# Optimization experiments

Hardware: AMD Instinct MI355X
Metric: run time of the kernel (lower is better)

Reference implementation:

```python
import jax, jax.numpy as jnp
import numpy as np
import math

B, C_IN, C_QK, H, W, NH = 1, 256, 128, 96, 96, 8
SCALE = math.sqrt(C_QK / NH)  # sqrt(planes/num_head) = 4.0
TEMP = 1.0


def conv1x1(x, w, b=None):
    # x: [B, Cin, H, W], w: [Cout, Cin] -> [B, Cout, H, W]
    y = jnp.einsum('bchw,oc->bohw', x, w)
    if b is not None:
        y = y + b[None, :, None, None]
    return y


def maxpool2x2(x):
    return jax.lax.reduce_window(x, -jnp.inf, jax.lax.max,
                                 (1, 1, 2, 2), (1, 1, 2, 2), 'VALID')


def setup_inputs() -> dict:
    key = jax.random.key(0)
    ks = jax.random.split(key, 5)
    x = jax.random.normal(ks[0], (B, C_IN, H, W), dtype=jnp.float32)
    # conv weights: init.normal_(w, 0, 0.01), zero bias; conv_value has no bias
    w_q = jax.random.normal(ks[1], (C_QK, C_IN), dtype=jnp.float32) * 0.01
    b_q = jnp.zeros((C_QK,), dtype=jnp.float32)
    w_k = jax.random.normal(ks[2], (C_QK, C_IN), dtype=jnp.float32) * 0.01
    b_k = jnp.zeros((C_QK,), dtype=jnp.float32)
    w_v = jax.random.normal(ks[3], (C_IN, C_IN), dtype=jnp.float32) * 0.01
    return {'x': x, 'w_q': w_q, 'b_q': b_q, 'w_k': w_k, 'b_k': b_k, 'w_v': w_v}


def reference(x, w_q, b_q, w_k, b_k, w_v):
    residual = x
    input_x = maxpool2x2(x)                       # [B, Cin, H/2, W/2]
    Hd, Wd = H // 2, W // 2
    Nq, Nk = H * W, Hd * Wd

    q = conv1x1(x, w_q, b_q)                      # [B, Cqk, H, W]
    k = conv1x1(input_x, w_k, b_k)                # [B, Cqk, Hd, Wd]
    v = conv1x1(input_x, w_v)                     # [B, Cin, Hd, Wd]

    dq = C_QK // NH
    dv = C_IN // NH
    q = q.reshape(B * NH, dq, Nq)
    k = k.reshape(B * NH, dq, Nk)
    v = v.reshape(B * NH, dv, Nk)

    # dot distance: scaled by sqrt(planes/num_head) and temp (nowd empty)
    sim = jnp.einsum('bdq,bdk->bqk', q, k) / (SCALE * TEMP)
    attn = jax.nn.softmax(sim, axis=2)            # softmax over keys

    # out = value @ attn^T  -> [B*NH, dv, Nq]
    out = jnp.einsum('bdk,bqk->bdq', v, attn)
    out = out.reshape(B, C_IN, H, W)
    return out + residual
```

## Files before the change

kernel.cpp:

```cpp
#include <hip/hip_runtime.h>
#include <hip/hip_bf16.h>
#include <math.h>

#define C_IN   256
#define C_QK   128
#define NH     8
#define H_     96
#define W_     96
#define NQ     (H_*W_)
#define HD     48
#define WD     48
#define NK     (HD*WD)
#define DQ     16
#define DV     32
#define NQC    (NQ/32)
#define NKC    (NK/32)
#define QPAIRS (NQC/2)
#define KQRT   (NKC/4)
#define KSTEPS (C_IN/16)
#define QS     0.3606737602222409f

typedef __attribute__((ext_vector_type(8)))  short short8v;
typedef __attribute__((ext_vector_type(16))) float f32x16;
typedef __attribute__((ext_vector_type(2)))  int   v2i;

union B8u { uint u[4]; short8v v; };

static __device__ inline ushort bf16r(float f) {
    __hip_bfloat16 h = __float2bfloat16(f);
    return *reinterpret_cast<ushort*>(&h);
}
static __device__ inline uint cvtpk(float lo, float hi) {
    uint r;
    asm("v_cvt_pk_bf16_f32 %0, %1, %2" : "=v"(r) : "v"(lo), "v"(hi));
    return r;
}
static __device__ inline void lswap(uint a, uint b, uint& x, uint& y, int hi) {
#if __has_builtin(__builtin_amdgcn_permlane32_swap)
    v2i r = __builtin_amdgcn_permlane32_swap((int)a, (int)b, false, false);
    x = (uint)r.x;
    y = (uint)r.y;
#else
    uint bx = (uint)__shfl_xor((int)b, 32);
    uint ax = (uint)__shfl_xor((int)a, 32);
    x = hi ? bx : a;
    y = hi ? b : ax;
#endif
}
static __device__ inline float fexp2(float v) {
#if __has_builtin(__builtin_amdgcn_exp2f)
    return __builtin_amdgcn_exp2f(v);
#else
    return __expf(v * 0.6931471805599453f);
#endif
}

#define U_XB   (NQC*KSTEPS*64)
#define U_XPB  (NKC*KSTEPS*64)
#define U_WQ   (4*KSTEPS*64)
#define U_WK   (4*KSTEPS*64)
#define U_WV   (8*KSTEPS*64)
#define U_FRAG (U_XB+U_XPB+U_WQ+U_WK+U_WV)
#define U_TOT  (U_FRAG + 128)

__global__ __launch_bounds__(256) void prep_kernel(
    const float* __restrict__ x,  const float* __restrict__ wq, const float* __restrict__ bq,
    const float* __restrict__ wk, const float* __restrict__ wv,
    ushort* __restrict__ xbP, ushort* __restrict__ xpbP,
    ushort* __restrict__ wqP, ushort* __restrict__ wkP, ushort* __restrict__ wvP,
    float* __restrict__ bqs)
{
    int t = blockIdx.x * 256 + threadIdx.x;
    if (t >= U_TOT) return;
    if (t >= U_FRAG) { int i = t - U_FRAG; bqs[i] = bq[i] * QS; return; }

    union { ushort s[8]; uint4 v; } ou;
    int u = t;
    if (u < U_XB) {
        int l = u & 63, rest = u >> 6;
        int ks = rest & 15, nc = rest >> 4;
        int n  = nc * 32 + (l & 31);
        int k0 = ks * 16 + 8 * (l >> 5);
        #pragma unroll
        for (int j = 0; j < 8; ++j) ou.s[j] = bf16r(x[(size_t)(k0 + j) * NQ + n]);
        *(uint4*)&xbP[(size_t)u * 8] = ou.v;
        return;
    }
    u -= U_XB;
    if (u < U_XPB) {
        int l = u & 63, rest = u >> 6;
        int ks = rest & 15, nc = rest >> 4;
        int np = nc * 32 + (l & 31);
        int k0 = ks * 16 + 8 * (l >> 5);
        int py = np / WD, px = np - py * WD;
        const float* base = x + (2 * py) * W_ + 2 * px;
        #pragma unroll
        for (int j = 0; j < 8; ++j) {
            const float* p = base + (size_t)(k0 + j) * NQ;
            ou.s[j] = bf16r(fmaxf(fmaxf(p[0], p[1]), fmaxf(p[W_], p[W_ + 1])));
        }
        *(uint4*)&xpbP[(size_t)u * 8] = ou.v;
        return;
    }
    u -= U_XPB;
    if (u < U_WQ) {
        int l = u & 63, ks = (u >> 6) & 15, mb = u >> 10;
        int m = mb * 32 + (l & 31), k0 = ks * 16 + 8 * (l >> 5);
        #pragma unroll
        for (int j = 0; j < 8; ++j) ou.s[j] = bf16r(wq[m * C_IN + k0 + j] * QS);
        *(uint4*)&wqP[(size_t)u * 8] = ou.v;
        return;
    }
    u -= U_WQ;
    if (u < U_WK) {
        int l = u & 63, ks = (u >> 6) & 15, mb = u >> 10;
        int m = mb * 32 + (l & 31), k0 = ks * 16 + 8 * (l >> 5);
        #pragma unroll
        for (int j = 0; j < 8; ++j) ou.s[j] = bf16r(wk[m * C_IN + k0 + j]);
        *(uint4*)&wkP[(size_t)u * 8] = ou.v;
        return;
    }
    u -= U_WK;
    {
        int l = u & 63, ks = (u >> 6) & 15, cb = u >> 10;
        int c = cb * 32 + (l & 31), k0 = ks * 16 + 8 * (l >> 5);
        #pragma unroll
        for (int j = 0; j < 8; ++j) ou.s[j] = bf16r(wv[c * C_IN + k0 + j]);
        *(uint4*)&wvP[(size_t)u * 8] = ou.v;
    }
}

static __device__ inline f32x16 mfma_loop(const ushort* __restrict__ A,
                                          const ushort* __restrict__ B) {
    f32x16 acc;
    #pragma unroll
    for (int r = 0; r < 16; ++r) acc[r] = 0.0f;
    #pragma unroll
    for (int s = 0; s < KSTEPS; ++s) {
        short8v a = *(const short8v*)(A + (size_t)s * 512);
        short8v b = *(const short8v*)(B + (size_t)s * 512);
        acc = __builtin_amdgcn_mfma_f32_32x32x16_bf16(a, b, acc, 0, 0, 0);
    }
    return acc;
}
static __device__ inline void xform(const f32x16& acc, int hi, short8v& F1, short8v& F2) {
    uint a0 = cvtpk(acc[0],  acc[1]),  a1 = cvtpk(acc[2],  acc[3]);
    uint b0 = cvtpk(acc[4],  acc[5]),  b1 = cvtpk(acc[6],  acc[7]);
    uint a2 = cvtpk(acc[8],  acc[9]),  a3 = cvtpk(acc[10], acc[11]);
    uint b2 = cvtpk(acc[12], acc[13]), b3 = cvtpk(acc[14], acc[15]);
    B8u f1, f2;
    lswap(a0, b0, f1.u[0], f1.u[2], hi);
    lswap(a1, b1, f1.u[1], f1.u[3], hi);
    lswap(a2, b2, f2.u[0], f2.u[2], hi);
    lswap(a3, b3, f2.u[1], f2.u[3], hi);
    F1 = f1.v; F2 = f2.v;
}

#define T_Q 1152
#define T_K (T_Q + 288)
#define T_ALL (T_K + 576)

__global__ __launch_bounds__(256) void gemm_fused(
    const ushort* __restrict__ xbP, const ushort* __restrict__ xpbP,
    const ushort* __restrict__ wqP, const ushort* __restrict__ wkP,
    const ushort* __restrict__ wvP,
    const float* __restrict__ bqs, const float* __restrict__ bk,
    ushort* __restrict__ qpack, ushort* __restrict__ kpack, ushort* __restrict__ vpack)
{
    int lane = threadIdx.x & 63, wvi = threadIdx.x >> 6;
    int hi = lane >> 5;
    int t = blockIdx.x * 4 + wvi;
    if (t >= T_ALL) return;

    if (t < T_Q) {
        int mb = t / NQC, nc = t - mb * NQC;
        const ushort* A = wqP + ((size_t)(mb * KSTEPS) * 64 + lane) * 8;
        const ushort* B = xbP + ((size_t)(nc * KSTEPS) * 64 + lane) * 8;
        f32x16 acc = mfma_loop(A, B);
        #pragma unroll
        for (int r = 0; r < 16; ++r)
            acc[r] += bqs[mb * 32 + (r & 3) + 8 * (r >> 2) + 4 * hi];
        short8v F1, F2;
        xform(acc, hi, F1, F2);
        *(short8v*)&qpack[((size_t)((2 * mb)     * NQC + nc) * 64 + lane) * 8] = F1;
        *(short8v*)&qpack[((size_t)((2 * mb + 1) * NQC + nc) * 64 + lane) * 8] = F2;
    } else if (t < T_K) {
        int t2 = t - T_Q;
        int mb = t2 / NKC, nc = t2 - mb * NKC;
        const ushort* A = wkP  + ((size_t)(mb * KSTEPS) * 64 + lane) * 8;
        const ushort* B = xpbP + ((size_t)(nc * KSTEPS) * 64 + lane) * 8;
        f32x16 acc = mfma_loop(A, B);
        #pragma unroll
        for (int r = 0; r < 16; ++r)
            acc[r] += bk[mb * 32 + (r & 3) + 8 * (r >> 2) + 4 * hi];
        short8v F1, F2;
        xform(acc, hi, F1, F2);
        *(short8v*)&kpack[((size_t)((2 * mb)     * NKC + nc) * 64 + lane) * 8] = F1;
        *(short8v*)&kpack[((size_t)((2 * mb + 1) * NKC + nc) * 64 + lane) * 8] = F2;
    } else {
        int t3 = t - T_K;
        int cb = t3 / NKC, kc = t3 - cb * NKC;
        const ushort* A = xpbP + ((size_t)(kc * KSTEPS) * 64 + lane) * 8;
        const ushort* B = wvP  + ((size_t)(cb * KSTEPS) * 64 + lane) * 8;
        f32x16 acc = mfma_loop(A, B);
        short8v F1, F2;
        xform(acc, hi, F1, F2);
        *(short8v*)&vpack[((size_t)((cb * NKC + kc) * 2 + 0) * 64 + lane) * 8] = F1;
        *(short8v*)&vpack[((size_t)((cb * NKC + kc) * 2 + 1) * 64 + lane) * 8] = F2;
    }
}

__global__ __launch_bounds__(256, 4) void attn_kernel(const ushort* __restrict__ qpack,
                                                      const ushort* __restrict__ kpack,
                                                      const ushort* __restrict__ vpack,
                                                      const float* __restrict__ x,
                                                      float* __restrict__ out) {
    __shared__ float part[4][2][64][20];
    const int h = blockIdx.y;
    const int tid = threadIdx.x, lane = tid & 63;
    const int kh = tid >> 6;
    const int q31 = lane & 31, hi = lane >> 5;
    const int qp = blockIdx.x;

    short8v qf0 = *(const short8v*)&qpack[((size_t)(h * NQC + 2 * qp)     * 64 + lane) * 8];
    short8v qf1 = *(const short8v*)&qpack[((size_t)(h * NQC + 2 * qp + 1) * 64 + lane) * 8];

    const ushort* kp = kpack + ((size_t)(h * NKC + kh * KQRT) * 64 + lane) * 8;
    const ushort* vp = vpack + ((size_t)(h * NKC + kh * KQRT) * 2 * 64 + lane) * 8;

    short8v kf = *(const short8v*)kp;
    short8v v0 = *(const short8v*)vp;
    short8v v1 = *(const short8v*)(vp + 512);

    f32x16 o0, o1, zc;
    #pragma unroll
    for (int r = 0; r < 16; ++r) { o0[r] = 0.0f; o1[r] = 0.0f; zc[r] = 0.0f; }
    float rs0 = 0.0f, rs1 = 0.0f;

    for (int c = 0; c < KQRT; ++c) {
        short8v kcur = kf, v0c = v0, v1c = v1;
        int cn = (c == KQRT - 1) ? 0 : (c + 1);
        kf = *(const short8v*)(kp + (size_t)cn * 512);
        v0 = *(const short8v*)(vp + (size_t)cn * 1024);
        v1 = *(const short8v*)(vp + (size_t)cn * 1024 + 512);

        {
            f32x16 s = __builtin_amdgcn_mfma_f32_32x32x16_bf16(kcur, qf0, zc, 0, 0, 0);
            float e[16];
            #pragma unroll
            for (int r = 0; r < 16; ++r) e[r] = fexp2(s[r]);
            float t0 = 0.0f;
            #pragma unroll
            for (int r = 0; r < 16; ++r) t0 += e[r];
            rs0 += t0;
            uint a0 = cvtpk(e[0],  e[1]),  a1 = cvtpk(e[2],  e[3]);
            uint b0 = cvtpk(e[4],  e[5]),  b1 = cvtpk(e[6],  e[7]);
            uint a2 = cvtpk(e[8],  e[9]),  a3 = cvtpk(e[10], e[11]);
            uint b2 = cvtpk(e[12], e[13]), b3 = cvtpk(e[14], e[15]);
            B8u B1, B2;
            lswap(a0, b0, B1.u[0], B1.u[2], hi);
            lswap(a1, b1, B1.u[1], B1.u[3], hi);
            lswap(a2, b2, B2.u[0], B2.u[2], hi);
            lswap(a3, b3, B2.u[1], B2.u[3], hi);
            o0 = __builtin_amdgcn_mfma_f32_32x32x16_bf16(v0c, B1.v, o0, 0, 0, 0);
            o0 = __builtin_amdgcn_mfma_f32_32x32x16_bf16(v1c, B2.v, o0, 0, 0, 0);
        }
        {
            f32x16 s = __builtin_amdgcn_mfma_f32_32x32x16_bf16(kcur, qf1, zc, 0, 0, 0);
            float e[16];
            #pragma unroll
            for (int r = 0; r < 16; ++r) e[r] = fexp2(s[r]);
            float t0 = 0.0f;
            #pragma unroll
            for (int r = 0; r < 16; ++r) t0 += e[r];
            rs1 += t0;
            uint a0 = cvtpk(e[0],  e[1]),  a1 = cvtpk(e[2],  e[3]);
            uint b0 = cvtpk(e[4],  e[5]),  b1 = cvtpk(e[6],  e[7]);
            uint a2 = cvtpk(e[8],  e[9]),  a3 = cvtpk(e[10], e[11]);
            uint b2 = cvtpk(e[12], e[13]), b3 = cvtpk(e[14], e[15]);
            B8u B1, B2;
            lswap(a0, b0, B1.u[0], B1.u[2], hi);
            lswap(a1, b1, B1.u[1], B1.u[3], hi);
            lswap(a2, b2, B2.u[0], B2.u[2], hi);
            lswap(a3, b3, B2.u[1], B2.u[3], hi);
            o1 = __builtin_amdgcn_mfma_f32_32x32x16_bf16(v0c, B1.v, o1, 0, 0, 0);
            o1 = __builtin_amdgcn_mfma_f32_32x32x16_bf16(v1c, B2.v, o1, 0, 0, 0);
        }
    }

    rs0 += __shfl_xor(rs0, 32);
    rs1 += __shfl_xor(rs1, 32);

    {
        float* p0 = &part[kh][0][lane][0];
        #pragma unroll
        for (int i = 0; i < 4; ++i)
            *(float4*)&p0[4 * i] = *(float4*)((const float*)&o0 + 4 * i);
        p0[16] = rs0;
        float* p1 = &part[kh][1][lane][0];
        #pragma unroll
        for (int i = 0; i < 4; ++i)
            *(float4*)&p1[4 * i] = *(float4*)((const float*)&o1 + 4 * i);
        p1[16] = rs1;
    }
    __syncthreads();

    if (kh < 2) {
        float o[16] = {};
        float rs = 0.0f;
        #pragma unroll
        for (int w = 0; w < 4; ++w) {
            const float* pw = &part[w][kh][lane][0];
            #pragma unroll
            for (int i = 0; i < 4; ++i) {
                float4 f = *(const float4*)&pw[4 * i];
                o[4 * i + 0] += f.x; o[4 * i + 1] += f.y;
                o[4 * i + 2] += f.z; o[4 * i + 3] += f.w;
            }
            rs += pw[16];
        }
        float inv = 1.0f / rs;
        int q = (2 * qp + kh) * 32 + q31;
        #pragma unroll
        for (int r = 0; r < 16; ++r) {
            int dv = (r & 3) + 8 * (r >> 2) + 4 * hi;
            size_t i0 = (size_t)(h * DV + dv) * NQ + q;
            out[i0] = o[r] * inv + x[i0];
        }
    }
}

extern "C" void kernel_launch(void* const* d_in, const int* in_sizes, int n_in,
                              void* d_out, int out_size, void* d_ws, size_t ws_size,
                              hipStream_t stream) {
    const float* x  = (const float*)d_in[0];
    const float* wq = (const float*)d_in[1];
    const float* bq = (const float*)d_in[2];
    const float* wk = (const float*)d_in[3];
    const float* bk = (const float*)d_in[4];
    const float* wv = (const float*)d_in[5];
    float* out = (float*)d_out;

    ushort* p = (ushort*)d_ws;
    ushort* xbP   = p;  p += (size_t)U_XB  * 8;
    ushort* xpbP  = p;  p += (size_t)U_XPB * 8;
    ushort* wqP   = p;  p += (size_t)U_WQ  * 8;
    ushort* wkP   = p;  p += (size_t)U_WK  * 8;
    ushort* wvP   = p;  p += (size_t)U_WV  * 8;
    ushort* qpack = p;  p += (size_t)NH * NQC * 64 * 8;
    ushort* kpack = p;  p += (size_t)NH * NKC * 64 * 8;
    ushort* vpack = p;  p += (size_t)NH * NKC * 2 * 64 * 8;
    float*  bqs   = (float*)p;

    prep_kernel<<<(U_TOT + 255) / 256, 256, 0, stream>>>(x, wq, bq, wk, wv,
                                                         xbP, xpbP, wqP, wkP, wvP, bqs);
    gemm_fused<<<(T_ALL + 3) / 4, 256, 0, stream>>>(xbP, xpbP, wqP, wkP, wvP,
                                                    bqs, bk, qpack, kpack, vpack);
    attn_kernel<<<dim3(QPAIRS, NH), 256, 0, stream>>>(qpack, kpack, vpack, x, out);
}
```

Baseline: 105.8 us.

## Fuse x bf16 conversion into Q projection and trim attention register pressure

The prep kernel no longer builds a packed bf16 copy of the full-resolution input. The Q-projection path in the fused GEMM now reads fp32 x directly, converts it to bf16 in registers and feeds the MFMA, which removes one full write and read of the input tensor. The attention kernel is also restructured: each softmax step is split into two half-batches of exponentials, the second value fragment is loaded inside the loop instead of prefetched, and the minimum-occupancy hint on the launch bounds is dropped. These attention changes aim to cut register pressure, but the v1 load now sits on the critical path, and the Q GEMM's strided fp32 loads may coalesce less well.

```diff
diff --git a/kernel.cpp b/kernel.cpp
--- a/kernel.cpp
+++ b/kernel.cpp
@@ -55,18 +55,17 @@
 #endif
 }
 
-#define U_XB   (NQC*KSTEPS*64)
 #define U_XPB  (NKC*KSTEPS*64)
 #define U_WQ   (4*KSTEPS*64)
 #define U_WK   (4*KSTEPS*64)
 #define U_WV   (8*KSTEPS*64)
-#define U_FRAG (U_XB+U_XPB+U_WQ+U_WK+U_WV)
+#define U_FRAG (U_XPB+U_WQ+U_WK+U_WV)
 #define U_TOT  (U_FRAG + 128)
 
 __global__ __launch_bounds__(256) void prep_kernel(
     const float* __restrict__ x,  const float* __restrict__ wq, const float* __restrict__ bq,
     const float* __restrict__ wk, const float* __restrict__ wv,
-    ushort* __restrict__ xbP, ushort* __restrict__ xpbP,
+    ushort* __restrict__ xpbP,
     ushort* __restrict__ wqP, ushort* __restrict__ wkP, ushort* __restrict__ wvP,
     float* __restrict__ bqs)
 {
@@ -76,17 +75,6 @@
 
     union { ushort s[8]; uint4 v; } ou;
     int u = t;
-    if (u < U_XB) {
-        int l = u & 63, rest = u >> 6;
-        int ks = rest & 15, nc = rest >> 4;
-        int n  = nc * 32 + (l & 31);
-        int k0 = ks * 16 + 8 * (l >> 5);
-        #pragma unroll
-        for (int j = 0; j < 8; ++j) ou.s[j] = bf16r(x[(size_t)(k0 + j) * NQ + n]);
-        *(uint4*)&xbP[(size_t)u * 8] = ou.v;
-        return;
-    }
-    u -= U_XB;
     if (u < U_XPB) {
         int l = u & 63, rest = u >> 6;
         int ks = rest & 15, nc = rest >> 4;
@@ -161,7 +149,7 @@
 #define T_ALL (T_K + 576)
 
 __global__ __launch_bounds__(256) void gemm_fused(
-    const ushort* __restrict__ xbP, const ushort* __restrict__ xpbP,
+    const float* __restrict__ x, const ushort* __restrict__ xpbP,
     const ushort* __restrict__ wqP, const ushort* __restrict__ wkP,
     const ushort* __restrict__ wvP,
     const float* __restrict__ bqs, const float* __restrict__ bk,
@@ -175,8 +163,21 @@
     if (t < T_Q) {
         int mb = t / NQC, nc = t - mb * NQC;
         const ushort* A = wqP + ((size_t)(mb * KSTEPS) * 64 + lane) * 8;
-        const ushort* B = xbP + ((size_t)(nc * KSTEPS) * 64 + lane) * 8;
-        f32x16 acc = mfma_loop(A, B);
+        const float* xb = x + (size_t)(8 * hi) * NQ + nc * 32 + (lane & 31);
+        f32x16 acc;
+        #pragma unroll
+        for (int r = 0; r < 16; ++r) acc[r] = 0.0f;
+        #pragma unroll
+        for (int s = 0; s < KSTEPS; ++s) {
+            float f[8];
+            #pragma unroll
+            for (int j = 0; j < 8; ++j) f[j] = xb[(size_t)(s * 16 + j) * NQ];
+            B8u bf;
+            #pragma unroll
+            for (int m = 0; m < 4; ++m) bf.u[m] = cvtpk(f[2 * m], f[2 * m + 1]);
+            short8v a = *(const short8v*)(A + (size_t)s * 512);
+            acc = __builtin_amdgcn_mfma_f32_32x32x16_bf16(a, bf.v, acc, 0, 0, 0);
+        }
         #pragma unroll
         for (int r = 0; r < 16; ++r)
             acc[r] += bqs[mb * 32 + (r & 3) + 8 * (r >> 2) + 4 * hi];
@@ -210,11 +211,38 @@
     }
 }
 
-__global__ __launch_bounds__(256, 4) void attn_kernel(const ushort* __restrict__ qpack,
-                                                      const ushort* __restrict__ kpack,
-                                                      const ushort* __restrict__ vpack,
-                                                      const float* __restrict__ x,
-                                                      float* __restrict__ out) {
+static __device__ inline void qstep(short8v kcur, short8v qf, short8v v0c, short8v v1c,
+                                    f32x16& o, float& rs, const f32x16& zc, int hi) {
+    f32x16 s = __builtin_amdgcn_mfma_f32_32x32x16_bf16(kcur, qf, zc, 0, 0, 0);
+    {
+        float e0 = fexp2(s[0]), e1 = fexp2(s[1]), e2 = fexp2(s[2]), e3 = fexp2(s[3]);
+        float e4 = fexp2(s[4]), e5 = fexp2(s[5]), e6 = fexp2(s[6]), e7 = fexp2(s[7]);
+        rs += ((e0 + e1) + (e2 + e3)) + ((e4 + e5) + (e6 + e7));
+        uint a0 = cvtpk(e0, e1), a1 = cvtpk(e2, e3);
+        uint b0 = cvtpk(e4, e5), b1 = cvtpk(e6, e7);
+        B8u B1;
+        lswap(a0, b0, B1.u[0], B1.u[2], hi);
+        lswap(a1, b1, B1.u[1], B1.u[3], hi);
+        o = __builtin_amdgcn_mfma_f32_32x32x16_bf16(v0c, B1.v, o, 0, 0, 0);
+    }
+    {
+        float e0 = fexp2(s[8]),  e1 = fexp2(s[9]),  e2 = fexp2(s[10]), e3 = fexp2(s[11]);
+        float e4 = fexp2(s[12]), e5 = fexp2(s[13]), e6 = fexp2(s[14]), e7 = fexp2(s[15]);
+        rs += ((e0 + e1) + (e2 + e3)) + ((e4 + e5) + (e6 + e7));
+        uint a0 = cvtpk(e0, e1), a1 = cvtpk(e2, e3);
+        uint b0 = cvtpk(e4, e5), b1 = cvtpk(e6, e7);
+        B8u B2;
+        lswap(a0, b0, B2.u[0], B2.u[2], hi);
+        lswap(a1, b1, B2.u[1], B2.u[3], hi);
+        o = __builtin_amdgcn_mfma_f32_32x32x16_bf16(v1c, B2.v, o, 0, 0, 0);
+    }
+}
+
+__global__ __launch_bounds__(256) void attn_kernel(const ushort* __restrict__ qpack,
+                                                   const ushort* __restrict__ kpack,
+                                                   const ushort* __restrict__ vpack,
+                                                   const float* __restrict__ x,
+                                                   float* __restrict__ out) {
     __shared__ float part[4][2][64][20];
     const int h = blockIdx.y;
     const int tid = threadIdx.x, lane = tid & 63;
@@ -230,7 +258,6 @@
 
     short8v kf = *(const short8v*)kp;
     short8v v0 = *(const short8v*)vp;
-    short8v v1 = *(const short8v*)(vp + 512);
 
     f32x16 o0, o1, zc;
     #pragma unroll
@@ -238,54 +265,14 @@
     float rs0 = 0.0f, rs1 = 0.0f;
 
     for (int c = 0; c < KQRT; ++c) {
-        short8v kcur = kf, v0c = v0, v1c = v1;
+        short8v kcur = kf, v0c = v0;
+        short8v v1c = *(const short8v*)(vp + (size_t)c * 1024 + 512);
         int cn = (c == KQRT - 1) ? 0 : (c + 1);
         kf = *(const short8v*)(kp + (size_t)cn * 512);
         v0 = *(const short8v*)(vp + (size_t)cn * 1024);
-        v1 = *(const short8v*)(vp + (size_t)cn * 1024 + 512);
-
-        {
-            f32x16 s = __builtin_amdgcn_mfma_f32_32x32x16_bf16(kcur, qf0, zc, 0, 0, 0);
-            float e[16];
-            #pragma unroll
-            for (int r = 0; r < 16; ++r) e[r] = fexp2(s[r]);
-            float t0 = 0.0f;
-            #pragma unroll
-            for (int r = 0; r < 16; ++r) t0 += e[r];
-            rs0 += t0;
-            uint a0 = cvtpk(e[0],  e[1]),  a1 = cvtpk(e[2],  e[3]);
-            uint b0 = cvtpk(e[4],  e[5]),  b1 = cvtpk(e[6],  e[7]);
-            uint a2 = cvtpk(e[8],  e[9]),  a3 = cvtpk(e[10], e[11]);
-            uint b2 = cvtpk(e[12], e[13]), b3 = cvtpk(e[14], e[15]);
-            B8u B1, B2;
-            lswap(a0, b0, B1.u[0], B1.u[2], hi);
-            lswap(a1, b1, B1.u[1], B1.u[3], hi);
-            lswap(a2, b2, B2.u[0], B2.u[2], hi);
-            lswap(a3, b3, B2.u[1], B2.u[3], hi);
-            o0 = __builtin_amdgcn_mfma_f32_32x32x16_bf16(v0c, B1.v, o0, 0, 0, 0);
-            o0 = __builtin_amdgcn_mfma_f32_32x32x16_bf16(v1c, B2.v, o0, 0, 0, 0);
-        }
-        {
-            f32x16 s = __builtin_amdgcn_mfma_f32_32x32x16_bf16(kcur, qf1, zc, 0, 0, 0);
-            float e[16];
-            #pragma unroll
-            for (int r = 0; r < 16; ++r) e[r] = fexp2(s[r]);
-            float t0 = 0.0f;
-            #pragma unroll
-            for (int r = 0; r < 16; ++r) t0 += e[r];
-            rs1 += t0;
-            uint a0 = cvtpk(e[0],  e[1]),  a1 = cvtpk(e[2],  e[3]);
-            uint b0 = cvtpk(e[4],  e[5]),  b1 = cvtpk(e[6],  e[7]);
-            uint a2 = cvtpk(e[8],  e[9]),  a3 = cvtpk(e[10], e[11]);
-            uint b2 = cvtpk(e[12], e[13]), b3 = cvtpk(e[14], e[15]);
-            B8u B1, B2;
-            lswap(a0, b0, B1.u[0], B1.u[2], hi);
-            lswap(a1, b1, B1.u[1], B1.u[3], hi);
-            lswap(a2, b2, B2.u[0], B2.u[2], hi);
-            lswap(a3, b3, B2.u[1], B2.u[3], hi);
-            o1 = __builtin_amdgcn_mfma_f32_32x32x16_bf16(v0c, B1.v, o1, 0, 0, 0);
-            o1 = __builtin_amdgcn_mfma_f32_32x32x16_bf16(v1c, B2.v, o1, 0, 0, 0);
-        }
+
+        qstep(kcur, qf0, v0c, v1c, o0, rs0, zc, hi);
+        qstep(kcur, qf1, v0c, v1c, o1, rs1, zc, hi);
     }
 
     rs0 += __shfl_xor(rs0, 32);
@@ -342,7 +329,6 @@
     float* out = (float*)d_out;
 
     ushort* p = (ushort*)d_ws;
-    ushort* xbP   = p;  p += (size_t)U_XB  * 8;
     ushort* xpbP  = p;  p += (size_t)U_XPB * 8;
     ushort* wqP   = p;  p += (size_t)U_WQ  * 8;
     ushort* wkP   = p;  p += (size_t)U_WK  * 8;
@@ -353,8 +339,8 @@
     float*  bqs   = (float*)p;
 
     prep_kernel<<<(U_TOT + 255) / 256, 256, 0, stream>>>(x, wq, bq, wk, wv,
-                                                         xbP, xpbP, wqP, wkP, wvP, bqs);
-    gemm_fused<<<(T_ALL + 3) / 4, 256, 0, stream>>>(xbP, xpbP, wqP, wkP, wvP,
+                                                         xpbP, wqP, wkP, wvP, bqs);
+    gemm_fused<<<(T_ALL + 3) / 4, 256, 0, stream>>>(x, xpbP, wqP, wkP, wvP,
                                                     bqs, bk, qpack, kpack, vpack);
     attn_kernel<<<dim3(QPAIRS, NH), 256, 0, stream>>>(qpack, kpack, vpack, x, out);
 }
```

After: 116.5 us. 1.1x slower.
